# Kernel tuning notes

Measured on AMD Instinct MI355X. Metric: run time of the kernel, lower is better.

## Reference

```python
import jax, jax.numpy as jnp
import numpy as np

NEG_SLOPE = 0.1

def lrelu(x):
    return jnp.where(x >= 0, x, NEG_SLOPE * x)

def conv1d(x, w, b, stride=2):
    # x: [N, C_in, W], w: [C_out, C_in, K], VALID padding, given stride
    y = jax.lax.conv_general_dilated(x, w, (stride,), 'VALID',
                                     dimension_numbers=('NCH', 'OIH', 'NCH'))
    return y + b[None, :, None]

def setup_inputs() -> dict:
    key = jax.random.key(0)
    ks = jax.random.split(key, 16)
    N_NODES = 50000
    N_EDGES = 4950000
    POS_C, CONV_C, CONV_W = 3, 3, 151
    HID, OUT = 256, 1
    W2 = 37  # width after two stride-2 k=3 convs on 151
    IN_G = POS_C + W2  # 40

    def lin_init(k, fan_out, fan_in):
        s = 1.0 / np.sqrt(fan_in)
        k1, k2 = jax.random.split(k)
        return (jax.random.uniform(k1, (fan_out, fan_in), jnp.float32, -s, s),
                jax.random.uniform(k2, (fan_out,), jnp.float32, -s, s))

    pose = jax.random.normal(ks[0], (N_NODES, POS_C), jnp.float32)
    views = jax.random.normal(ks[1], (N_NODES, CONV_C, CONV_W), jnp.float32)
    edge_index = jax.random.randint(ks[2], (2, N_EDGES), 0, N_NODES, jnp.int64)

    # encoder1: Conv1d(3 -> 9, k=3, s=2); encoder2: Conv1d(9 -> 1, k=3, s=2)
    s1 = 1.0 / np.sqrt(CONV_C * 3)
    w_e1 = jax.random.uniform(ks[3], (CONV_C ** 2, CONV_C, 3), jnp.float32, -s1, s1)
    b_e1 = jax.random.uniform(ks[4], (CONV_C ** 2,), jnp.float32, -s1, s1)
    s2 = 1.0 / np.sqrt(CONV_C ** 2 * 3)
    w_e2 = jax.random.uniform(ks[5], (1, CONV_C ** 2, 3), jnp.float32, -s2, s2)
    b_e2 = jax.random.uniform(ks[6], (1,), jnp.float32, -s2, s2)

    # GraphConv: lin_rel (with bias) on aggregated neighbors, lin_root (no bias) on self
    w_rel, b_rel = lin_init(ks[7], HID, IN_G)
    w_root, _ = lin_init(ks[8], HID, IN_G)

    w_l1, b_l1 = lin_init(ks[9], HID, HID)
    w_l2, b_l2 = lin_init(ks[10], HID, HID)
    w_l3, b_l3 = lin_init(ks[11], HID, HID)
    w_pred, b_pred = lin_init(ks[12], OUT, HID)

    return dict(pose=pose, views=views, edge_index=edge_index,
                w_e1=w_e1, b_e1=b_e1, w_e2=w_e2, b_e2=b_e2,
                w_rel=w_rel, b_rel=b_rel, w_root=w_root,
                w_l1=w_l1, b_l1=b_l1, w_l2=w_l2, b_l2=b_l2,
                w_l3=w_l3, b_l3=b_l3, w_pred=w_pred, b_pred=b_pred)

def reference(pose, views, edge_index, w_e1, b_e1, w_e2, b_e2,
              w_rel, b_rel, w_root,
              w_l1, b_l1, w_l2, b_l2, w_l3, b_l3, w_pred, b_pred):
    n_nodes = pose.shape[0]
    # view encoder
    v = lrelu(conv1d(views, w_e1, b_e1))          # [N, 9, 75]
    v = lrelu(conv1d(v, w_e2, b_e2))              # [N, 1, 37]
    x = jnp.concatenate([pose, v[:, 0, :]], axis=1)  # [N, 40]
    # GraphConv (aggr='add'): out = lin_rel(sum_{j->i} x_j) + lin_root(x_i)
    src, dst = edge_index[0], edge_index[1]
    agg = jax.ops.segment_sum(x[src], dst, num_segments=n_nodes)  # [N, 40]
    h = lrelu(agg @ w_rel.T + b_rel + x @ w_root.T)               # [N, 256]
    # MLP stack (dropout is identity in eval mode)
    h = lrelu(h @ w_l1.T + b_l1)
    h = lrelu(h @ w_l2.T + b_l2)
    h = lrelu(h @ w_l3.T + b_l3)
    return h @ w_pred.T + b_pred  # [N, 1]
```

## Files before the change

kernel.cpp:

```cpp
#include <hip/hip_runtime.h>
#include <hip/hip_fp16.h>

#define NEG_SLOPE 0.1f
__device__ __forceinline__ float lrelu(float v) { return fmaxf(v, NEG_SLOPE * v); }

constexpr int CAP = 8704;
constexpr int EPB = 8192;

typedef __attribute__((ext_vector_type(8))) short short8;
typedef __attribute__((ext_vector_type(4))) float f32x4;
typedef __attribute__((ext_vector_type(2))) float f32x2;
typedef __attribute__((ext_vector_type(4))) int i32x4;

__device__ __forceinline__ unsigned short f2bf(float f) {
    union { float f; unsigned u; } v; v.f = f;
    const unsigned r = v.u + 0x7FFF + ((v.u >> 16) & 1);
    return (unsigned short)(r >> 16);
}
__device__ __forceinline__ float bf2f(unsigned short h) {
    union { unsigned u; float f; } v; v.u = ((unsigned)h) << 16;
    return v.f;
}

__global__ __launch_bounds__(256) void encoder_kernel(
        const float* __restrict__ pose,
        const float* __restrict__ views,
        const float* __restrict__ w1, const float* __restrict__ b1,
        const float* __restrict__ w2, const float* __restrict__ b2,
        const float* __restrict__ w_l1, const float* __restrict__ w_l2,
        const float* __restrict__ w_l3, const float* __restrict__ w_rel,
        const float* __restrict__ w_root,
        unsigned short* __restrict__ Wb1, unsigned short* __restrict__ Wb2,
        unsigned short* __restrict__ Wb3, unsigned short* __restrict__ Wg,
        int* __restrict__ gcur,
        unsigned short* __restrict__ xHi, unsigned short* __restrict__ xLo,
        __half* __restrict__ xh, int N)
{
    __shared__ float s_w1[81];
    __shared__ float s_b1[9];
    __shared__ float s_w2[27];
    __shared__ float s_b2[1];
    __shared__ float s_c1[4][9][80];

    const int t = threadIdx.x;

    if (blockIdx.x < 256) {
        const int i = blockIdx.x * 256 + t;
        Wb1[i] = f2bf(w_l1[i]);
        Wb2[i] = f2bf(w_l2[i]);
        Wb3[i] = f2bf(w_l3[i]);
        if (i < 40960) {
            const int m = i / 160, c = i % 160;
            const int k = c % 80;
            const float v = (k < 40) ? w_rel[m * 40 + k] : w_root[m * 40 + (k - 40)];
            Wg[i] = f2bf(v);
        }
        if (i < 1024) gcur[i] = 0;
        if (i < 40) xh[(size_t)N * 40 + i] = __float2half(0.f);
    }

    if (t < 81) s_w1[t] = w1[t];
    if (t >= 96 && t < 105) s_b1[t - 96] = b1[t - 96];
    if (t >= 128 && t < 155) s_w2[t - 128] = w2[t - 128];
    if (t == 240) s_b2[0] = b2[0];
    __syncthreads();

    const int nb = blockIdx.x * 4;

    #pragma unroll
    for (int pass = 0; pass < 2; pass++) {
        const int task = pass * 256 + t;
        if (task < 300) {
            const int ln = task / 75;
            const int p  = task % 75;
            const int n  = min(nb + ln, N - 1);
            const float* __restrict__ vin = views + (size_t)n * 453 + 2 * p;
            float e[3], o[3], e1[3];
            #pragma unroll
            for (int ic = 0; ic < 3; ic++) {
                const float* ci = vin + ic * 151;
                e[ic] = ci[0]; o[ic] = ci[1]; e1[ic] = ci[2];
            }
            const int didx = (p & 1) * 40 + (p >> 1);
            #pragma unroll
            for (int oc = 0; oc < 9; oc++) {
                float v = s_b1[oc];
                #pragma unroll
                for (int ic = 0; ic < 3; ic++)
                    v += s_w1[oc * 9 + ic * 3 + 0] * e[ic]
                       + s_w1[oc * 9 + ic * 3 + 1] * o[ic]
                       + s_w1[oc * 9 + ic * 3 + 2] * e1[ic];
                s_c1[ln][oc][didx] = lrelu(v);
            }
        }
    }
    __syncthreads();

    if (t < 160) {
        const int ln = t / 40, f = t % 40;
        const int n  = min(nb + ln, N - 1);
        float outv;
        if (f < 3) {
            outv = pose[(size_t)n * 3 + f];
        } else {
            const int ow = f - 3;
            float v = s_b2[0];
            #pragma unroll
            for (int ic = 0; ic < 9; ic++)
                v += s_w2[ic * 3 + 0] * s_c1[ln][ic][ow]
                   + s_w2[ic * 3 + 1] * s_c1[ln][ic][40 + ow]
                   + s_w2[ic * 3 + 2] * s_c1[ln][ic][ow + 1];
            outv = lrelu(v);
        }
        const unsigned short hi = f2bf(outv);
        const unsigned short lo = f2bf(outv - bf2f(hi));
        xHi[(size_t)n * 40 + f] = hi;
        xLo[(size_t)n * 40 + f] = lo;
        xh[(size_t)n * 40 + f] = __float2half(outv);
    }
}

__global__ __launch_bounds__(512) void bin_kernel(
        const int* __restrict__ ei, int* __restrict__ gcur,
        int* __restrict__ pairs, int E, int NB)
{
    __shared__ int s_hist[1024];
    __shared__ int s_loff[1024];
    __shared__ int s_base[1024];
    __shared__ int s_wave8[8];
    __shared__ int s_pk[EPB];
    __shared__ unsigned short s_bkt[EPB];
    const int t = threadIdx.x;
    const int lane = t & 63, wid = t >> 6;
    const int e0 = blockIdx.x * EPB + t * 16;
    const int tot = min(E - (int)blockIdx.x * EPB, EPB);

    for (int i = t; i < 1024; i += 512) s_hist[i] = 0;
    __syncthreads();

    int pk[16], mt[16];
    auto proc = [&](int j, int sv, int dv) {
        const int b = dv >> 6;
        const int r = atomicAdd(&s_hist[b], 1);
        pk[j] = sv | ((dv & 63) << 22);
        mt[j] = b | (r << 10);
    };

    if (e0 + 16 <= E) {
        #pragma unroll
        for (int q = 0; q < 4; q++) {
            const int4 sv = *(const int4*)(ei + e0 + 4 * q);
            const int4 dv = *(const int4*)(ei + E + e0 + 4 * q);
            proc(4 * q + 0, sv.x, dv.x);
            proc(4 * q + 1, sv.y, dv.y);
            proc(4 * q + 2, sv.z, dv.z);
            proc(4 * q + 3, sv.w, dv.w);
        }
    } else {
        #pragma unroll
        for (int j = 0; j < 16; j++) {
            mt[j] = -1;
            const int e = e0 + j;
            if (e < E) proc(j, ei[e], ei[E + e]);
        }
    }
    __syncthreads();

    int carry = 0;
    #pragma unroll
    for (int base = 0; base < 1024; base += 512) {
        const int i = base + t;
        const int v = s_hist[i];
        int sc = v;
        #pragma unroll
        for (int d = 1; d < 64; d <<= 1) {
            const int u = __shfl_up(sc, d);
            if (lane >= d) sc += u;
        }
        if (lane == 63) s_wave8[wid] = sc;
        __syncthreads();
        if (wid == 0) {
            int wv = (lane < 8) ? s_wave8[lane] : 0;
            #pragma unroll
            for (int d = 1; d < 8; d <<= 1) {
                const int u = __shfl_up(wv, d);
                if (lane >= d) wv += u;
            }
            if (lane < 8) s_wave8[lane] = wv;
        }
        __syncthreads();
        const int waveoff = (wid > 0) ? s_wave8[wid - 1] : 0;
        s_loff[i] = carry + waveoff + sc - v;
        const int chunk_tot = s_wave8[7];
        __syncthreads();
        carry += chunk_tot;
    }

    for (int i = t; i < NB; i += 512) {
        const int c = s_hist[i];
        if (c > 0) s_base[i] = atomicAdd(&gcur[i], c);
    }
    __syncthreads();

    #pragma unroll
    for (int j = 0; j < 16; j++) {
        if (mt[j] >= 0) {
            const int b = mt[j] & 1023;
            const int pos = s_loff[b] + (mt[j] >> 10);
            s_pk[pos] = pk[j];
            s_bkt[pos] = (unsigned short)b;
        }
    }
    __syncthreads();

    for (int i = t; i < tot; i += 512) {
        const int b = s_bkt[i];
        const int p = s_base[b] + (i - s_loff[b]);
        if (p < CAP) pairs[b * CAP + p] = s_pk[i];
    }
}

__device__ __forceinline__ int aswz(int row, int col) {
    return row * 256 + (col ^ ((row & 7) << 3));
}

__device__ __forceinline__ void gload16(const void* g, void* l) {
    __builtin_amdgcn_global_load_lds(
        (const __attribute__((address_space(1))) unsigned int*)g,
        (__attribute__((address_space(3))) unsigned int*)l,
        16, 0, 0);
}

__device__ __forceinline__ void stage_panel(const unsigned short* __restrict__ W,
                                            int wstride, int k0,
                                            unsigned short* buf, int wave, int lane)
{
    const int rbase = wave * 32 + (lane >> 2);
    const int cu = (((lane & 3) ^ ((lane >> 3) & 3))) * 8;
    #pragma unroll
    for (int j = 0; j < 2; j++) {
        const int row = rbase + j * 16;
        gload16(W + (size_t)row * wstride + k0 + cu,
                buf + (wave * 2 + j) * 512);
    }
}

__device__ __forceinline__ void gemm_layer(const unsigned short* __restrict__ aT,
                                           const unsigned short* __restrict__ W,
                                           int wstride, int K,
                                           unsigned short* __restrict__ sWb,
                                           int wave, int lane, int l16, int q,
                                           f32x4 acc[4][2])
{
    const int NP = K >> 5;
    stage_panel(W, wstride, 0,  sWb,        wave, lane);
    stage_panel(W, wstride, 32, sWb + 8192, wave, lane);
    const int wro = (wave * 2) * 512 + l16 * 32 + (q ^ ((l16 >> 1) & 3)) * 8;

    for (int p = 0; p < NP; p++) {
        unsigned short* wb = sWb + (p & 1) * 8192;
        if (p + 1 < NP) asm volatile("s_waitcnt vmcnt(2)" ::: "memory");
        else            asm volatile("s_waitcnt vmcnt(0)" ::: "memory");
        short8 af[4], wf[2];
        #pragma unroll
        for (int nt = 0; nt < 4; nt++)
            af[nt] = *(const short8*)(aT + aswz(nt * 16 + l16, p * 32 + q * 8));
        #pragma unroll
        for (int mt = 0; mt < 2; mt++)
            wf[mt] = *(const short8*)(wb + wro + mt * 512);
        if (p + 2 < NP) {
            asm volatile("s_waitcnt lgkmcnt(0)" ::: "memory");
            __builtin_amdgcn_sched_barrier(0);
            stage_panel(W, wstride, (p + 2) * 32, wb, wave, lane);
        }
        #pragma unroll
        for (int nt = 0; nt < 4; nt++)
            #pragma unroll
            for (int mt = 0; mt < 2; mt++)
                acc[nt][mt] = __builtin_amdgcn_mfma_f32_16x16x32_bf16(af[nt], wf[mt], acc[nt][mt], 0, 0, 0);
    }
}

__device__ __forceinline__ void epi_to_lds(f32x4 acc[4][2], const float* __restrict__ b,
                                           unsigned short* __restrict__ aT,
                                           int wave, int l16, int q)
{
    float bias[2];
    #pragma unroll
    for (int mt = 0; mt < 2; mt++) bias[mt] = b[wave * 32 + mt * 16 + l16];
    #pragma unroll
    for (int nt = 0; nt < 4; nt++)
        #pragma unroll
        for (int r = 0; r < 4; r++)
            #pragma unroll
            for (int mt = 0; mt < 2; mt++) {
                const int row = nt * 16 + q * 4 + r;
                const int col = wave * 32 + mt * 16 + l16;
                aT[aswz(row, col)] = f2bf(lrelu(acc[nt][mt][r] + bias[mt]));
            }
}

__global__ __launch_bounds__(512) void sg_gemm_kernel(
        const int* __restrict__ gcur,
        const int* __restrict__ pairs,
        const __half* __restrict__ xh,
        const unsigned short* __restrict__ xHi,
        const unsigned short* __restrict__ xLo,
        const unsigned short* __restrict__ Wg,
        const float* __restrict__ b_rel,
        const unsigned short* __restrict__ Wb1,
        const float* __restrict__ b_l1,
        const unsigned short* __restrict__ Wb2,
        const float* __restrict__ b_l2,
        const unsigned short* __restrict__ Wb3,
        const float* __restrict__ b_l3,
        const float* __restrict__ w_pred,
        const float* __restrict__ b_pred,
        float* __restrict__ out, int N)
{
    __shared__ __align__(16) unsigned short aT[64 * 256];
    __shared__ __align__(16) char uni[32768];
    unsigned short* s_sorted = (unsigned short*)uni;
    int* s_cnt = (int*)(uni + 17408);
    int* s_off = (int*)(uni + 17664);
    unsigned short* sWb = (unsigned short*)uni;

    const int b = blockIdx.x;
    const int t = threadIdx.x;
    const int n0 = b * 64;
    const int wave = t >> 6, lane = t & 63, q = lane >> 4, l16 = lane & 15;
    const int cnt = min(gcur[b], CAP);
    const int* __restrict__ pr = pairs + (size_t)b * CAP;

    if (t < 64) s_cnt[t] = 0;

    int pk[17];
    {
        const i32x4* __restrict__ pr4 = (const i32x4*)pr;
        #pragma unroll
        for (int j = 0; j < 4; j++) {
            const int m = t + j * 512;
            const i32x4 v = __builtin_nontemporal_load(pr4 + m);
            const int e0 = m * 4;
            pk[4 * j + 0] = (e0 + 0 < cnt) ? v.x : -1;
            pk[4 * j + 1] = (e0 + 1 < cnt) ? v.y : -1;
            pk[4 * j + 2] = (e0 + 2 < cnt) ? v.z : -1;
            pk[4 * j + 3] = (e0 + 3 < cnt) ? v.w : -1;
        }
        const int m16 = 8192 + t;
        pk[16] = (m16 < cnt) ? __builtin_nontemporal_load(pr + m16) : -1;
    }
    for (int u = t; u < 640; u += 512) {
        const int row = u / 10, c = (u % 10) * 4;
        const int srow = min(n0 + row, N - 1);
        const size_t off = (size_t)srow * 40 + c;
        *(ushort4*)(aT + aswz(row, 40 + c))  = *(const ushort4*)(xHi + off);
        *(ushort4*)(aT + aswz(row, 120 + c)) = *(const ushort4*)(xLo + off);
    }
    __syncthreads();

    int rk[17];
    #pragma unroll
    for (int j = 0; j < 17; j++)
        if (pk[j] >= 0) rk[j] = atomicAdd(&s_cnt[pk[j] >> 22], 1);
    __syncthreads();

    if (t < 64) {
        const int c = s_cnt[t];
        const int p = ((c + 23) / 24) * 24;
        int sc = p;
        #pragma unroll
        for (int d = 1; d < 64; d <<= 1) {
            const int u = __shfl_up(sc, d);
            if (t >= d) sc += u;
        }
        s_off[t] = sc - p;
    }
    __syncthreads();

    if (t < 64) {
        const int e0 = s_off[t] + s_cnt[t];
        const int e1 = s_off[t] + ((s_cnt[t] + 23) / 24) * 24;
        for (int i = e0; i < e1 && i < CAP; i++) s_sorted[i] = (unsigned short)N;
    }
    #pragma unroll
    for (int j = 0; j < 17; j++) {
        if (pk[j] >= 0) {
            const int pos = s_off[pk[j] >> 22] + rk[j];
            if (pos < CAP) s_sorted[pos] = (unsigned short)(pk[j] & 0xFFFF);
        }
    }
    __syncthreads();

    {
        const int slot = min(lane / 5, 11);
        const int f8 = lane % 5;
        const char* __restrict__ xb = (const char*)xh + f8 * 16;

        #pragma unroll 1
        for (int i = 0; i < 8; i++) {
            const int ln = wave * 8 + i;
            const int n = n0 + ln;
            if (n >= N) break;
            const int c = s_cnt[ln];
            const int cntp = ((c + 23) / 24) * 24;
            const unsigned short* __restrict__ srt = s_sorted + s_off[ln] + slot;

            f32x2 a0 = {0.f, 0.f}, a1 = {0.f, 0.f}, a2 = {0.f, 0.f}, a3 = {0.f, 0.f};
            union { unsigned v; __half2 h; } cv;
            auto cv2 = [&](unsigned u) -> f32x2 {
                cv.v = u;
                const float2 ff = __half22float2(cv.h);
                f32x2 r; r.x = ff.x; r.y = ff.y; return r;
            };
            auto acc8 = [&](uint4 u) {
                a0 += cv2(u.x); a1 += cv2(u.y); a2 += cv2(u.z); a3 += cv2(u.w);
            };

            int e = 0;
            #pragma unroll 1
            for (; e + 48 <= cntp; e += 48) {
                const int o0 = srt[e] * 80;
                const int o1 = srt[e + 12] * 80;
                const int o2 = srt[e + 24] * 80;
                const int o3 = srt[e + 36] * 80;
                const uint4 u0 = *(const uint4*)(xb + o0);
                const uint4 u1 = *(const uint4*)(xb + o1);
                const uint4 u2 = *(const uint4*)(xb + o2);
                const uint4 u3 = *(const uint4*)(xb + o3);
                acc8(u0); acc8(u1); acc8(u2); acc8(u3);
            }
            if (e < cntp) {
                const int o0 = srt[e] * 80;
                const int o1 = srt[e + 12] * 80;
                const uint4 u0 = *(const uint4*)(xb + o0);
                const uint4 u1 = *(const uint4*)(xb + o1);
                acc8(u0); acc8(u1);
            }

            #pragma unroll
            for (int st = 0; st < 2; st++) {
                const int d = st ? 15 : 30;
                a0.x += __shfl(a0.x, lane + d); a0.y += __shfl(a0.y, lane + d);
                a1.x += __shfl(a1.x, lane + d); a1.y += __shfl(a1.y, lane + d);
                a2.x += __shfl(a2.x, lane + d); a2.y += __shfl(a2.y, lane + d);
                a3.x += __shfl(a3.x, lane + d); a3.y += __shfl(a3.y, lane + d);
            }
            a0.x += __shfl(a0.x, lane + 5) + __shfl(a0.x, lane + 10);
            a0.y += __shfl(a0.y, lane + 5) + __shfl(a0.y, lane + 10);
            a1.x += __shfl(a1.x, lane + 5) + __shfl(a1.x, lane + 10);
            a1.y += __shfl(a1.y, lane + 5) + __shfl(a1.y, lane + 10);
            a2.x += __shfl(a2.x, lane + 5) + __shfl(a2.x, lane + 10);
            a2.y += __shfl(a2.y, lane + 5) + __shfl(a2.y, lane + 10);
            a3.x += __shfl(a3.x, lane + 5) + __shfl(a3.x, lane + 10);
            a3.y += __shfl(a3.y, lane + 5) + __shfl(a3.y, lane + 10);

            if (lane < 5) {
                const float av[8] = {a0.x, a0.y, a1.x, a1.y, a2.x, a2.y, a3.x, a3.y};
                unsigned short h[8], l[8];
                #pragma unroll
                for (int j = 0; j < 8; j++) {
                    h[j] = f2bf(av[j]);
                    l[j] = f2bf(av[j] - bf2f(h[j]));
                }
                uint4 H, L;
                H.x = h[0] | ((unsigned)h[1] << 16); H.y = h[2] | ((unsigned)h[3] << 16);
                H.z = h[4] | ((unsigned)h[5] << 16); H.w = h[6] | ((unsigned)h[7] << 16);
                L.x = l[0] | ((unsigned)l[1] << 16); L.y = l[2] | ((unsigned)l[3] << 16);
                L.z = l[4] | ((unsigned)l[5] << 16); L.w = l[6] | ((unsigned)l[7] << 16);
                *(uint4*)(aT + aswz(ln, lane * 8))      = H;
                *(uint4*)(aT + aswz(ln, 80 + lane * 8)) = L;
            }
        }
    }
    __syncthreads();

    {
        f32x4 acc[4][2] = {};
        gemm_layer(aT, Wg, 160, 160, sWb, wave, lane, l16, q, acc);
        __syncthreads();
        epi_to_lds(acc, b_rel, aT, wave, l16, q);
        __syncthreads();
    }
    {
        f32x4 acc[4][2] = {};
        gemm_layer(aT, Wb1, 256, 256, sWb, wave, lane, l16, q, acc);
        __syncthreads();
        epi_to_lds(acc, b_l1, aT, wave, l16, q);
        __syncthreads();
    }
    {
        f32x4 acc[4][2] = {};
        gemm_layer(aT, Wb2, 256, 256, sWb, wave, lane, l16, q, acc);
        __syncthreads();
        epi_to_lds(acc, b_l2, aT, wave, l16, q);
        __syncthreads();
    }
    {
        f32x4 acc[4][2] = {};
        gemm_layer(aT, Wb3, 256, 256, sWb, wave, lane, l16, q, acc);

        float bias[2], wp[2];
        #pragma unroll
        for (int mt = 0; mt < 2; mt++) {
            const int col = wave * 32 + mt * 16 + l16;
            bias[mt] = b_l3[col];
            wp[mt] = w_pred[col];
        }
        float* spw = (float*)(uni + wave * 2048);
        #pragma unroll
        for (int nt = 0; nt < 4; nt++)
            #pragma unroll
            for (int r = 0; r < 4; r++) {
                float p = 0.f;
                #pragma unroll
                for (int mt = 0; mt < 2; mt++)
                    p += lrelu(acc[nt][mt][r] + bias[mt]) * wp[mt];
                p += __shfl_xor(p, 1);
                p += __shfl_xor(p, 2);
                p += __shfl_xor(p, 4);
                p += __shfl_xor(p, 8);
                if (l16 == 0) spw[nt * 16 + q * 4 + r] = p;
            }
        __syncthreads();

        if (t < 64) {
            const int row = n0 + t;
            if (row < N) {
                float s = b_pred[0];
                #pragma unroll
                for (int w = 0; w < 8; w++)
                    s += ((const float*)(uni + w * 2048))[t];
                out[row] = s;
            }
        }
    }
}

extern "C" void kernel_launch(void* const* d_in, const int* in_sizes, int n_in,
                              void* d_out, int out_size, void* d_ws, size_t ws_size,
                              hipStream_t stream)
{
    const float* pose   = (const float*)d_in[0];
    const float* views  = (const float*)d_in[1];
    const int*   ei     = (const int*)d_in[2];
    const float* w_e1   = (const float*)d_in[3];
    const float* b_e1   = (const float*)d_in[4];
    const float* w_e2   = (const float*)d_in[5];
    const float* b_e2   = (const float*)d_in[6];
    const float* w_rel  = (const float*)d_in[7];
    const float* b_rel  = (const float*)d_in[8];
    const float* w_root = (const float*)d_in[9];
    const float* w_l1   = (const float*)d_in[10];
    const float* b_l1   = (const float*)d_in[11];
    const float* w_l2   = (const float*)d_in[12];
    const float* b_l2   = (const float*)d_in[13];
    const float* w_l3   = (const float*)d_in[14];
    const float* b_l3   = (const float*)d_in[15];
    const float* w_pred = (const float*)d_in[16];
    const float* b_pred = (const float*)d_in[17];
    float* out = (float*)d_out;

    const int N = in_sizes[0] / 3;
    const int E = in_sizes[2] / 2;
    const int NB = (N + 63) >> 6;

    unsigned short* xHi = (unsigned short*)d_ws;
    unsigned short* xLo = xHi + (size_t)N * 40;
    __half* xh = (__half*)(xLo + (size_t)N * 40);
    int* pairs = (int*)(xh + (size_t)(N + 1) * 40 + 24);
    int* gcur  = pairs + (size_t)NB * CAP;
    unsigned short* Wb1 = (unsigned short*)(gcur + 1024);
    unsigned short* Wb2 = Wb1 + 256 * 256;
    unsigned short* Wb3 = Wb2 + 256 * 256;
    unsigned short* Wg  = Wb3 + 256 * 256;

    encoder_kernel<<<(N + 3) / 4, 256, 0, stream>>>(
        pose, views, w_e1, b_e1, w_e2, b_e2,
        w_l1, w_l2, w_l3, w_rel, w_root,
        Wb1, Wb2, Wb3, Wg, gcur, xHi, xLo, xh, N);

    bin_kernel<<<(E + EPB - 1) / EPB, 512, 0, stream>>>(ei, gcur, pairs, E, NB);

    sg_gemm_kernel<<<NB, 512, 0, stream>>>(
        gcur, pairs, xh, xHi, xLo, Wg, b_rel,
        Wb1, b_l1, Wb2, b_l2, Wb3, b_l3,
        w_pred, b_pred, out, N);
}
```

Measured before the change: 323.4 us.

## Merge encoder and edge binning into one launch, split weight prep out

Weight conversion and counter reset move into a small prep kernel. The view encoder and the edge-binning pass are merged into one horizontally fused kernel whose block index picks the role, so the two independent stages can run at the same time on the GPU. Encoder blocks now cover 8 nodes with 512 threads. The risk is that every block reserves the binning path's ~60KB of shared memory, which limits how many encoder blocks fit on a CU.

```diff
diff --git a/kernel.cpp b/kernel.cpp
--- a/kernel.cpp
+++ b/kernel.cpp
@@ -22,201 +22,209 @@
     return v.f;
 }
 
-__global__ __launch_bounds__(256) void encoder_kernel(
-        const float* __restrict__ pose,
-        const float* __restrict__ views,
-        const float* __restrict__ w1, const float* __restrict__ b1,
-        const float* __restrict__ w2, const float* __restrict__ b2,
+__device__ __forceinline__ f32x2 cv2(unsigned u) {
+    union { unsigned v; __half2 h; } cv; cv.v = u;
+    const float2 ff = __half22float2(cv.h);
+    f32x2 r; r.x = ff.x; r.y = ff.y; return r;
+}
+
+__global__ __launch_bounds__(256) void prep_kernel(
         const float* __restrict__ w_l1, const float* __restrict__ w_l2,
         const float* __restrict__ w_l3, const float* __restrict__ w_rel,
         const float* __restrict__ w_root,
         unsigned short* __restrict__ Wb1, unsigned short* __restrict__ Wb2,
         unsigned short* __restrict__ Wb3, unsigned short* __restrict__ Wg,
-        int* __restrict__ gcur,
+        int* __restrict__ gcur, __half* __restrict__ xh, int N)
+{
+    const int i = blockIdx.x * 256 + threadIdx.x;
+    Wb1[i] = f2bf(w_l1[i]);
+    Wb2[i] = f2bf(w_l2[i]);
+    Wb3[i] = f2bf(w_l3[i]);
+    if (i < 40960) {
+        const int m = i / 160, c = i % 160;
+        const int k = c % 80;
+        const float v = (k < 40) ? w_rel[m * 40 + k] : w_root[m * 40 + (k - 40)];
+        Wg[i] = f2bf(v);
+    }
+    if (i < 1024) gcur[i] = 0;
+    if (i < 40) xh[(size_t)N * 40 + i] = __float2half(0.f);
+}
+
+__global__ __launch_bounds__(512) void enc_bin_kernel(
+        const float* __restrict__ pose,
+        const float* __restrict__ views,
+        const float* __restrict__ w1, const float* __restrict__ b1,
+        const float* __restrict__ w2, const float* __restrict__ b2,
         unsigned short* __restrict__ xHi, unsigned short* __restrict__ xLo,
-        __half* __restrict__ xh, int N)
-{
-    __shared__ float s_w1[81];
-    __shared__ float s_b1[9];
-    __shared__ float s_w2[27];
-    __shared__ float s_b2[1];
-    __shared__ float s_c1[4][9][80];
-
-    const int t = threadIdx.x;
-
-    if (blockIdx.x < 256) {
-        const int i = blockIdx.x * 256 + t;
-        Wb1[i] = f2bf(w_l1[i]);
-        Wb2[i] = f2bf(w_l2[i]);
-        Wb3[i] = f2bf(w_l3[i]);
-        if (i < 40960) {
-            const int m = i / 160, c = i % 160;
-            const int k = c % 80;
-            const float v = (k < 40) ? w_rel[m * 40 + k] : w_root[m * 40 + (k - 40)];
-            Wg[i] = f2bf(v);
-        }
-        if (i < 1024) gcur[i] = 0;
-        if (i < 40) xh[(size_t)N * 40 + i] = __float2half(0.f);
-    }
-
-    if (t < 81) s_w1[t] = w1[t];
-    if (t >= 96 && t < 105) s_b1[t - 96] = b1[t - 96];
-    if (t >= 128 && t < 155) s_w2[t - 128] = w2[t - 128];
-    if (t == 240) s_b2[0] = b2[0];
-    __syncthreads();
-
-    const int nb = blockIdx.x * 4;
-
-    #pragma unroll
-    for (int pass = 0; pass < 2; pass++) {
-        const int task = pass * 256 + t;
-        if (task < 300) {
-            const int ln = task / 75;
-            const int p  = task % 75;
-            const int n  = min(nb + ln, N - 1);
-            const float* __restrict__ vin = views + (size_t)n * 453 + 2 * p;
-            float e[3], o[3], e1[3];
-            #pragma unroll
-            for (int ic = 0; ic < 3; ic++) {
-                const float* ci = vin + ic * 151;
-                e[ic] = ci[0]; o[ic] = ci[1]; e1[ic] = ci[2];
-            }
-            const int didx = (p & 1) * 40 + (p >> 1);
-            #pragma unroll
-            for (int oc = 0; oc < 9; oc++) {
-                float v = s_b1[oc];
-                #pragma unroll
-                for (int ic = 0; ic < 3; ic++)
-                    v += s_w1[oc * 9 + ic * 3 + 0] * e[ic]
-                       + s_w1[oc * 9 + ic * 3 + 1] * o[ic]
-                       + s_w1[oc * 9 + ic * 3 + 2] * e1[ic];
-                s_c1[ln][oc][didx] = lrelu(v);
-            }
-        }
-    }
-    __syncthreads();
-
-    if (t < 160) {
-        const int ln = t / 40, f = t % 40;
-        const int n  = min(nb + ln, N - 1);
-        float outv;
-        if (f < 3) {
-            outv = pose[(size_t)n * 3 + f];
-        } else {
-            const int ow = f - 3;
-            float v = s_b2[0];
-            #pragma unroll
-            for (int ic = 0; ic < 9; ic++)
-                v += s_w2[ic * 3 + 0] * s_c1[ln][ic][ow]
-                   + s_w2[ic * 3 + 1] * s_c1[ln][ic][40 + ow]
-                   + s_w2[ic * 3 + 2] * s_c1[ln][ic][ow + 1];
-            outv = lrelu(v);
-        }
-        const unsigned short hi = f2bf(outv);
-        const unsigned short lo = f2bf(outv - bf2f(hi));
-        xHi[(size_t)n * 40 + f] = hi;
-        xLo[(size_t)n * 40 + f] = lo;
-        xh[(size_t)n * 40 + f] = __float2half(outv);
-    }
-}
-
-__global__ __launch_bounds__(512) void bin_kernel(
+        __half* __restrict__ xh,
         const int* __restrict__ ei, int* __restrict__ gcur,
-        int* __restrict__ pairs, int E, int NB)
-{
-    __shared__ int s_hist[1024];
-    __shared__ int s_loff[1024];
-    __shared__ int s_base[1024];
-    __shared__ int s_wave8[8];
-    __shared__ int s_pk[EPB];
-    __shared__ unsigned short s_bkt[EPB];
+        int* __restrict__ pairs, int E, int NB, int NBB, int N)
+{
+    __shared__ __align__(16) char smem[61472];
     const int t = threadIdx.x;
     const int lane = t & 63, wid = t >> 6;
-    const int e0 = blockIdx.x * EPB + t * 16;
-    const int tot = min(E - (int)blockIdx.x * EPB, EPB);
-
-    for (int i = t; i < 1024; i += 512) s_hist[i] = 0;
-    __syncthreads();
-
-    int pk[16], mt[16];
-    auto proc = [&](int j, int sv, int dv) {
-        const int b = dv >> 6;
-        const int r = atomicAdd(&s_hist[b], 1);
-        pk[j] = sv | ((dv & 63) << 22);
-        mt[j] = b | (r << 10);
-    };
-
-    if (e0 + 16 <= E) {
-        #pragma unroll
-        for (int q = 0; q < 4; q++) {
-            const int4 sv = *(const int4*)(ei + e0 + 4 * q);
-            const int4 dv = *(const int4*)(ei + E + e0 + 4 * q);
-            proc(4 * q + 0, sv.x, dv.x);
-            proc(4 * q + 1, sv.y, dv.y);
-            proc(4 * q + 2, sv.z, dv.z);
-            proc(4 * q + 3, sv.w, dv.w);
+
+    if (blockIdx.x < (unsigned)NBB) {
+        int* s_hist = (int*)smem;
+        int* s_loff = (int*)(smem + 4096);
+        int* s_base = (int*)(smem + 8192);
+        int* s_wave8 = (int*)(smem + 12288);
+        int* s_pk = (int*)(smem + 12320);
+        unsigned short* s_bkt = (unsigned short*)(smem + 45088);
+
+        const int bbi = blockIdx.x;
+        const int e0 = bbi * EPB + t * 16;
+        const int tot = min(E - bbi * EPB, EPB);
+
+        for (int i = t; i < 1024; i += 512) s_hist[i] = 0;
+        __syncthreads();
+
+        int pk[16], mt[16];
+        auto proc = [&](int j, int sv, int dv) {
+            const int b = dv >> 6;
+            const int r = atomicAdd(&s_hist[b], 1);
+            pk[j] = sv | ((dv & 63) << 22);
+            mt[j] = b | (r << 10);
+        };
+
+        if (e0 + 16 <= E) {
+            #pragma unroll
+            for (int qq = 0; qq < 4; qq++) {
+                const int4 sv = *(const int4*)(ei + e0 + 4 * qq);
+                const int4 dv = *(const int4*)(ei + E + e0 + 4 * qq);
+                proc(4 * qq + 0, sv.x, dv.x);
+                proc(4 * qq + 1, sv.y, dv.y);
+                proc(4 * qq + 2, sv.z, dv.z);
+                proc(4 * qq + 3, sv.w, dv.w);
+            }
+        } else {
+            #pragma unroll
+            for (int j = 0; j < 16; j++) {
+                mt[j] = -1;
+                const int e = e0 + j;
+                if (e < E) proc(j, ei[e], ei[E + e]);
+            }
+        }
+        __syncthreads();
+
+        int carry = 0;
+        #pragma unroll
+        for (int base = 0; base < 1024; base += 512) {
+            const int i = base + t;
+            const int v = s_hist[i];
+            int sc = v;
+            #pragma unroll
+            for (int d = 1; d < 64; d <<= 1) {
+                const int u = __shfl_up(sc, d);
+                if (lane >= d) sc += u;
+            }
+            if (lane == 63) s_wave8[wid] = sc;
+            __syncthreads();
+            if (wid == 0) {
+                int wv = (lane < 8) ? s_wave8[lane] : 0;
+                #pragma unroll
+                for (int d = 1; d < 8; d <<= 1) {
+                    const int u = __shfl_up(wv, d);
+                    if (lane >= d) wv += u;
+                }
+                if (lane < 8) s_wave8[lane] = wv;
+            }
+            __syncthreads();
+            const int waveoff = (wid > 0) ? s_wave8[wid - 1] : 0;
+            s_loff[i] = carry + waveoff + sc - v;
+            const int chunk_tot = s_wave8[7];
+            __syncthreads();
+            carry += chunk_tot;
+        }
+
+        for (int i = t; i < NB; i += 512) {
+            const int c = s_hist[i];
+            if (c > 0) s_base[i] = atomicAdd(&gcur[i], c);
+        }
+        __syncthreads();
+
+        #pragma unroll
+        for (int j = 0; j < 16; j++) {
+            if (mt[j] >= 0) {
+                const int b = mt[j] & 1023;
+                const int pos = s_loff[b] + (mt[j] >> 10);
+                s_pk[pos] = pk[j];
+                s_bkt[pos] = (unsigned short)b;
+            }
+        }
+        __syncthreads();
+
+        for (int i = t; i < tot; i += 512) {
+            const int b = s_bkt[i];
+            const int p = s_base[b] + (i - s_loff[b]);
+            if (p < CAP) pairs[b * CAP + p] = s_pk[i];
         }
     } else {
-        #pragma unroll
-        for (int j = 0; j < 16; j++) {
-            mt[j] = -1;
-            const int e = e0 + j;
-            if (e < E) proc(j, ei[e], ei[E + e]);
-        }
-    }
-    __syncthreads();
-
-    int carry = 0;
-    #pragma unroll
-    for (int base = 0; base < 1024; base += 512) {
-        const int i = base + t;
-        const int v = s_hist[i];
-        int sc = v;
-        #pragma unroll
-        for (int d = 1; d < 64; d <<= 1) {
-            const int u = __shfl_up(sc, d);
-            if (lane >= d) sc += u;
-        }
-        if (lane == 63) s_wave8[wid] = sc;
-        __syncthreads();
-        if (wid == 0) {
-            int wv = (lane < 8) ? s_wave8[lane] : 0;
-            #pragma unroll
-            for (int d = 1; d < 8; d <<= 1) {
-                const int u = __shfl_up(wv, d);
-                if (lane >= d) wv += u;
-            }
-            if (lane < 8) s_wave8[lane] = wv;
-        }
-        __syncthreads();
-        const int waveoff = (wid > 0) ? s_wave8[wid - 1] : 0;
-        s_loff[i] = carry + waveoff + sc - v;
-        const int chunk_tot = s_wave8[7];
-        __syncthreads();
-        carry += chunk_tot;
-    }
-
-    for (int i = t; i < NB; i += 512) {
-        const int c = s_hist[i];
-        if (c > 0) s_base[i] = atomicAdd(&gcur[i], c);
-    }
-    __syncthreads();
-
-    #pragma unroll
-    for (int j = 0; j < 16; j++) {
-        if (mt[j] >= 0) {
-            const int b = mt[j] & 1023;
-            const int pos = s_loff[b] + (mt[j] >> 10);
-            s_pk[pos] = pk[j];
-            s_bkt[pos] = (unsigned short)b;
-        }
-    }
-    __syncthreads();
-
-    for (int i = t; i < tot; i += 512) {
-        const int b = s_bkt[i];
-        const int p = s_base[b] + (i - s_loff[b]);
-        if (p < CAP) pairs[b * CAP + p] = s_pk[i];
+        float* s_w1 = (float*)smem;
+        float* s_b1 = (float*)(smem + 336);
+        float* s_w2 = (float*)(smem + 384);
+        float* s_b2 = (float*)(smem + 496);
+        float (*s_c1)[9][80] = (float (*)[9][80])(smem + 512);
+
+        if (t < 81) s_w1[t] = w1[t];
+        if (t >= 96 && t < 105) s_b1[t - 96] = b1[t - 96];
+        if (t >= 128 && t < 155) s_w2[t - 128] = w2[t - 128];
+        if (t == 240) s_b2[0] = b2[0];
+        __syncthreads();
+
+        const int nb = (blockIdx.x - NBB) * 8;
+
+        #pragma unroll
+        for (int pass = 0; pass < 2; pass++) {
+            const int task = pass * 512 + t;
+            if (task < 600) {
+                const int ln = task / 75;
+                const int p  = task % 75;
+                const int n  = min(nb + ln, N - 1);
+                const float* __restrict__ vin = views + (size_t)n * 453 + 2 * p;
+                float e[3], o[3], e1[3];
+                #pragma unroll
+                for (int ic = 0; ic < 3; ic++) {
+                    const float* ci = vin + ic * 151;
+                    e[ic] = ci[0]; o[ic] = ci[1]; e1[ic] = ci[2];
+                }
+                const int didx = (p & 1) * 40 + (p >> 1);
+                #pragma unroll
+                for (int oc = 0; oc < 9; oc++) {
+                    float v = s_b1[oc];
+                    #pragma unroll
+                    for (int ic = 0; ic < 3; ic++)
+                        v += s_w1[oc * 9 + ic * 3 + 0] * e[ic]
+                           + s_w1[oc * 9 + ic * 3 + 1] * o[ic]
+                           + s_w1[oc * 9 + ic * 3 + 2] * e1[ic];
+                    s_c1[ln][oc][didx] = lrelu(v);
+                }
+            }
+        }
+        __syncthreads();
+
+        if (t < 320) {
+            const int ln = t / 40, f = t % 40;
+            const int n  = min(nb + ln, N - 1);
+            float outv;
+            if (f < 3) {
+                outv = pose[(size_t)n * 3 + f];
+            } else {
+                const int ow = f - 3;
+                float v = s_b2[0];
+                #pragma unroll
+                for (int ic = 0; ic < 9; ic++)
+                    v += s_w2[ic * 3 + 0] * s_c1[ln][ic][ow]
+                       + s_w2[ic * 3 + 1] * s_c1[ln][ic][40 + ow]
+                       + s_w2[ic * 3 + 2] * s_c1[ln][ic][ow + 1];
+                outv = lrelu(v);
+            }
+            const unsigned short hi = f2bf(outv);
+            const unsigned short lo = f2bf(outv - bf2f(hi));
+            xHi[(size_t)n * 40 + f] = hi;
+            xLo[(size_t)n * 40 + f] = lo;
+            xh[(size_t)n * 40 + f] = __float2half(outv);
+        }
     }
 }
 
@@ -407,12 +415,6 @@
             const unsigned short* __restrict__ srt = s_sorted + s_off[ln] + slot;
 
             f32x2 a0 = {0.f, 0.f}, a1 = {0.f, 0.f}, a2 = {0.f, 0.f}, a3 = {0.f, 0.f};
-            union { unsigned v; __half2 h; } cv;
-            auto cv2 = [&](unsigned u) -> f32x2 {
-                cv.v = u;
-                const float2 ff = __half22float2(cv.h);
-                f32x2 r; r.x = ff.x; r.y = ff.y; return r;
-            };
             auto acc8 = [&](uint4 u) {
                 a0 += cv2(u.x); a1 += cv2(u.y); a2 += cv2(u.z); a3 += cv2(u.w);
             };
@@ -564,6 +566,8 @@
     const int N = in_sizes[0] / 3;
     const int E = in_sizes[2] / 2;
     const int NB = (N + 63) >> 6;
+    const int NBB = (E + EPB - 1) / EPB;
+    const int NBE = (N + 7) / 8;
 
     unsigned short* xHi = (unsigned short*)d_ws;
     unsigned short* xLo = xHi + (size_t)N * 40;
@@ -575,12 +579,14 @@
     unsigned short* Wb3 = Wb2 + 256 * 256;
     unsigned short* Wg  = Wb3 + 256 * 256;
 
-    encoder_kernel<<<(N + 3) / 4, 256, 0, stream>>>(
+    prep_kernel<<<256, 256, 0, stream>>>(
+        w_l1, w_l2, w_l3, w_rel, w_root,
+        Wb1, Wb2, Wb3, Wg, gcur, xh, N);
+
+    enc_bin_kernel<<<NBB + NBE, 512, 0, stream>>>(
         pose, views, w_e1, b_e1, w_e2, b_e2,
-        w_l1, w_l2, w_l3, w_rel, w_root,
-        Wb1, Wb2, Wb3, Wg, gcur, xHi, xLo, xh, N);
-
-    bin_kernel<<<(E + EPB - 1) / EPB, 512, 0, stream>>>(ei, gcur, pairs, E, NB);
+        xHi, xLo, xh,
+        ei, gcur, pairs, E, NB, NBB, N);
 
     sg_gemm_kernel<<<NB, 512, 0, stream>>>(
         gcur, pairs, xh, xHi, xLo, Wg, b_rel,
```

Result: slower. 334.5 us (+3.4%).
